# Kernel optimization log

Hardware: AMD Instinct MI355X
Metric: run time of the kernel (lower is better)

Reference implementation:

```python
import jax, jax.numpy as jnp
import numpy as np

B, S, D, H = 2, 2048, 1024, 16
HD = D // H
BAND_LOWER, BAND_UPPER = -1, 0  # tf.linalg.band_part args -> causal


def _causal_add_mask(seq_len):
    # 1 - band_part(ones, lower, upper); 1 where attention is DISALLOWED
    i = jnp.arange(seq_len)[:, None]
    j = jnp.arange(seq_len)[None, :]
    keep = jnp.ones((seq_len, seq_len), bool)
    if BAND_LOWER >= 0:
        keep = keep & ((i - j) <= BAND_LOWER)
    if BAND_UPPER >= 0:
        keep = keep & ((j - i) <= BAND_UPPER)
    return 1.0 - keep.astype(jnp.float32)


def setup_inputs() -> dict:
    key = jax.random.key(0)
    ks = jax.random.split(key, 5)
    scale = 1.0 / np.sqrt(D)
    return {
        "x": jax.random.normal(ks[0], (B, S, D), jnp.float32),
        "wq": jax.random.normal(ks[1], (D, D), jnp.float32) * scale,
        "bq": jnp.zeros((D,), jnp.float32),
        "wk": jax.random.normal(ks[2], (D, D), jnp.float32) * scale,
        "bk": jnp.zeros((D,), jnp.float32),
        "wv": jax.random.normal(ks[3], (D, D), jnp.float32) * scale,
        "bv": jnp.zeros((D,), jnp.float32),
        "wo": jax.random.normal(ks[4], (D, D), jnp.float32) * scale,
        "bo": jnp.zeros((D,), jnp.float32),
    }


def _split_heads(t):
    # [B, S, D] -> [B, H, S, HD]
    return t.reshape(B, S, H, HD).transpose(0, 2, 1, 3)


def reference(x, wq, bq, wk, bk, wv, bv, wo, bo):
    q = _split_heads(x @ wq + bq)
    k = _split_heads(x @ wk + bk)
    v = _split_heads(x @ wv + bv)
    mask = _causal_add_mask(S)  # [S, S], 1 where masked
    logits = jnp.einsum("bhqd,bhkd->bhqk", q, k) / jnp.sqrt(
        jnp.asarray(HD, jnp.float32)
    )
    logits = logits + mask * -1e9
    attn = jax.nn.softmax(logits, axis=-1)
    out = jnp.einsum("bhqk,bhkd->bhqd", attn, v)  # [B, H, S, HD]
    out = out.transpose(0, 2, 1, 3).reshape(B, S, D)
    return out @ wo + bo
```

## Files before the change

kernel.cpp:

```cpp
#include <hip/hip_runtime.h>

#define S_  2048
#define D_  1024
#define H_  16
#define HD_ 64
#define M_  4096
#define K_  1024
#define NEL 4194304

typedef short  bf16x8 __attribute__((ext_vector_type(8)));
typedef float  f32x4  __attribute__((ext_vector_type(4)));
typedef float  f32x16 __attribute__((ext_vector_type(16)));
typedef unsigned int   u32;
typedef unsigned int   u32x4v __attribute__((ext_vector_type(4)));
typedef unsigned short u16;
typedef unsigned short u16x4 __attribute__((ext_vector_type(4)));

#define MFMA16(c,a,b) (c) = __builtin_amdgcn_mfma_f32_16x16x32_bf16((a),(b),(c),0,0,0)
#define MFMA32(c,a,b) (c) = __builtin_amdgcn_mfma_f32_32x32x16_bf16((a),(b),(c),0,0,0)

#define QSCALE 0.18033688011112042f

__device__ __forceinline__ u16 f2bf(float f) {
    union { float f; unsigned u; } v; v.f = f;
    unsigned u = v.u;
    u += 0x7FFFu + ((u >> 16) & 1u);
    return (u16)(u >> 16);
}

__device__ __forceinline__ u32 cvtpk(float lo, float hi) {
    u32 r;
    asm("v_cvt_pk_bf16_f32 %0, %1, %2" : "=v"(r) : "v"(lo), "v"(hi));
    return r;
}

__device__ __forceinline__ void gload16(const void* g, void* l) {
    __builtin_amdgcn_global_load_lds(
        (const __attribute__((address_space(1))) unsigned*)g,
        (__attribute__((address_space(3))) unsigned*)l, 16, 0, 0);
}

__global__ __launch_bounds__(256) void cvt_x(const float* __restrict__ x,
                                             u16* __restrict__ xb) {
    const int i = (blockIdx.x * 256 + threadIdx.x) * 8;
    f32x4 a = *(const f32x4*)&x[i];
    f32x4 b = *(const f32x4*)&x[i + 4];
    u16 t[8];
#pragma unroll
    for (int j = 0; j < 4; ++j) { t[j] = f2bf(a[j]); t[4 + j] = f2bf(b[j]); }
    *(bf16x8*)&xb[i] = *(const bf16x8*)t;
}

__global__ __launch_bounds__(256) void cvt_w(const float* __restrict__ w0,
                                             const float* __restrict__ w1,
                                             const float* __restrict__ w2,
                                             const float* __restrict__ w3,
                                             u16* __restrict__ Wt) {
    __shared__ float T[64][65];
    const float* W = blockIdx.z == 0 ? w0 : blockIdx.z == 1 ? w1
                   : blockIdx.z == 2 ? w2 : w3;
    const int k0 = blockIdx.x * 64, n0 = blockIdx.y * 64;
    const int r  = threadIdx.x >> 2, c0 = (threadIdx.x & 3) * 16;
#pragma unroll
    for (int j = 0; j < 4; ++j)
        *(f32x4*)&T[r][c0 + j * 4] = *(const f32x4*)&W[(size_t)(k0 + r) * D_ + n0 + c0 + j * 4];
    __syncthreads();
    u16 tmp[16];
#pragma unroll
    for (int j = 0; j < 16; ++j) tmp[j] = f2bf(T[c0 + j][r]);
    u16* dst = Wt + ((size_t)blockIdx.z * 1024 + n0 + r) * K_ + k0 + c0;
    *(bf16x8*)dst       = *(const bf16x8*)tmp;
    *(bf16x8*)(dst + 8) = *(const bf16x8*)(tmp + 8);
}

template <int BM, int MODE>
__global__ __launch_bounds__(256) void gemm2(
    const u16* __restrict__ A, const u16* __restrict__ Bt,
    const float* __restrict__ bias, void* __restrict__ Out)
{
    __shared__ u16 As[BM * 32];
    __shared__ u16 Bs[128 * 32];
    const int tid = threadIdx.x, lane = tid & 63, wid = tid >> 6;
    const int lr = lane & 15, lg = lane >> 4;
    const int n0 = blockIdx.x * 128, m0 = blockIdx.y * BM;
    const int wm = (wid >> 1) * (BM / 2), wn = (wid & 1) * 64;
    const int lrow = lane >> 2, lch = lane & 3;

    f32x4 acc[BM / 32][4] = {};

    for (int k0 = 0; k0 < K_; k0 += 32) {
        __syncthreads();
#pragma unroll
        for (int t = 0; t < BM / 64; ++t) {
            const int row = wid * (BM / 4) + t * 16 + lrow;
            gload16(A + (size_t)(m0 + row) * K_ + k0 + lch * 8,
                    (u16*)As + row * 32 + lch * 8);
        }
#pragma unroll
        for (int t = 0; t < 2; ++t) {
            const int row = wid * 32 + t * 16 + lrow;
            gload16(Bt + (size_t)(n0 + row) * K_ + k0 + lch * 8,
                    (u16*)Bs + row * 32 + lch * 8);
        }
        __syncthreads();

        bf16x8 af[BM / 32], bf[4];
#pragma unroll
        for (int i = 0; i < BM / 32; ++i)
            af[i] = *(const bf16x8*)&As[(wm + i * 16 + lr) * 32 + lg * 8];
#pragma unroll
        for (int j = 0; j < 4; ++j)
            bf[j] = *(const bf16x8*)&Bs[(wn + j * 16 + lr) * 32 + lg * 8];
#pragma unroll
        for (int i = 0; i < BM / 32; ++i)
#pragma unroll
            for (int j = 0; j < 4; ++j) MFMA16(acc[i][j], af[i], bf[j]);
    }

#pragma unroll
    for (int i = 0; i < BM / 32; ++i) {
#pragma unroll
        for (int j = 0; j < 4; ++j) {
            const int n = n0 + wn + j * 16 + lr;
            const float bv = bias[n];
            const int m = m0 + wm + i * 16 + lg * 4;
            if constexpr (MODE == 0) {
                u16* qkv = (u16*)Out;
                const int which = n >> 10, nn = n & 1023;
                const int h = nn >> 6, hd = nn & 63;
                const int b = m >> 11, s = m & 2047;
                if (which == 2) {
                    u16x4 pk;
#pragma unroll
                    for (int r4 = 0; r4 < 4; ++r4) pk[r4] = f2bf(acc[i][j][r4] + bv);
                    *(u16x4*)&qkv[(size_t)2 * NEL +
                                  ((size_t)(b * H_ + h) * HD_ + hd) * S_ + s] = pk;
                } else {
                    const float sc = (which == 0) ? QSCALE : 1.0f;
                    const size_t bas = (size_t)which * NEL + (size_t)(b * H_ + h) * S_ * HD_;
#pragma unroll
                    for (int r4 = 0; r4 < 4; ++r4)
                        qkv[bas + (size_t)(s + r4) * HD_ + hd] =
                            f2bf((acc[i][j][r4] + bv) * sc);
                }
            } else {
                float* o = (float*)Out;
#pragma unroll
                for (int r4 = 0; r4 < 4; ++r4)
                    o[(size_t)(m + r4) * D_ + n] = acc[i][j][r4] + bv;
            }
        }
    }
}

__global__ __launch_bounds__(128) void attn5(
    const u16* __restrict__ Q, const u16* __restrict__ K,
    const u16* __restrict__ Vt, u16* __restrict__ CTX)
{
    __shared__ float OB[64][33];
    __shared__ float MB[64], LB[64];

    const int tid  = threadIdx.x;
    const int lane = tid & 63, wv = tid >> 6;
    const int lo = lane & 31, hi = lane >> 5;
    const int idx = blockIdx.x;
    const int bh  = idx & 31;
    const int qb  = 63 - (idx >> 5);
    const int wq0 = qb * 32;
    const size_t base  = (size_t)bh * S_ * HD_;
    const size_t vbase = (size_t)bh * HD_ * S_;

    bf16x8 qf[4];
#pragma unroll
    for (int ks = 0; ks < 4; ++ks)
        qf[ks] = *(const bf16x8*)&Q[base + (size_t)(wq0 + lo) * HD_ + ks * 16 + hi * 8];

    f32x16 acc[2] = {};
    float m_ = -1e30f, l_ = 0.f;
    const int nt = (wq0 >> 6) + 1;

    for (int t = wv; t < nt; t += 2) {
        const int kv0 = t * 64;
        const bool sub1 = (kv0 + 32 <= wq0 + 31);

        f32x16 cT[2];
#pragma unroll
        for (int i = 0; i < 16; ++i) { cT[0][i] = 0.f; cT[1][i] = 0.f; }
        __builtin_amdgcn_s_setprio(1);
#pragma unroll
        for (int ks = 0; ks < 4; ++ks) {
            bf16x8 kf = *(const bf16x8*)&K[base + (size_t)(kv0 + lo) * HD_ + ks * 16 + hi * 8];
            MFMA32(cT[0], kf, qf[ks]);
        }
        if (sub1) {
#pragma unroll
            for (int ks = 0; ks < 4; ++ks) {
                bf16x8 kf = *(const bf16x8*)&K[base + (size_t)(kv0 + 32 + lo) * HD_ + ks * 16 + hi * 8];
                MFMA32(cT[1], kf, qf[ks]);
            }
        }
        __builtin_amdgcn_s_setprio(0);

        bf16x8 vf[2][4];
#pragma unroll
        for (int dt = 0; dt < 2; ++dt)
#pragma unroll
            for (int ks = 0; ks < 4; ++ks)
                if (ks < 2 || sub1)
                    vf[dt][ks] = *(const bf16x8*)&Vt[vbase + (size_t)(dt * 32 + lo) * S_ +
                                                     kv0 + ks * 16 + hi * 8];

        if (kv0 + 63 > wq0) {
            const int qg = wq0 + lo;
#pragma unroll
            for (int tt = 0; tt < 2; ++tt)
#pragma unroll
                for (int r = 0; r < 16; ++r) {
                    const int kvg = kv0 + tt * 32 + (r & 3) + 8 * (r >> 2) + 4 * hi;
                    if (kvg > qg) cT[tt][r] = -1e9f;
                }
        }

        float m8[8];
#pragma unroll
        for (int i = 0; i < 8; ++i)
            m8[i] = fmaxf(fmaxf(cT[0][i], cT[0][i + 8]), fmaxf(cT[1][i], cT[1][i + 8]));
        float mx = fmaxf(fmaxf(fmaxf(m8[0], m8[1]), fmaxf(m8[2], m8[3])),
                         fmaxf(fmaxf(m8[4], m8[5]), fmaxf(m8[6], m8[7])));
        mx = fmaxf(mx, __shfl_xor(mx, 32));

        if (!__all(mx <= m_ + 11.5f)) {
            const float mn = fmaxf(m_, mx);
            const float al = exp2f(m_ - mn);
            m_ = mn; l_ *= al;
            float alr[16];
#pragma unroll
            for (int r = 0; r < 16; ++r)
                alr[r] = __shfl(al, (r & 3) + 8 * (r >> 2) + 4 * hi);
#pragma unroll
            for (int r = 0; r < 16; ++r) { acc[0][r] *= alr[r]; acc[1][r] *= alr[r]; }
        }

#pragma unroll
        for (int i = 0; i < 16; ++i) {
            cT[0][i] = exp2f(cT[0][i] - m_);
            cT[1][i] = exp2f(cT[1][i] - m_);
        }
        float s8[8];
#pragma unroll
        for (int i = 0; i < 8; ++i)
            s8[i] = (cT[0][i] + cT[0][i + 8]) + (cT[1][i] + cT[1][i + 8]);
        float ssum = ((s8[0] + s8[1]) + (s8[2] + s8[3])) +
                     ((s8[4] + s8[5]) + (s8[6] + s8[7]));
        ssum += __shfl_xor(ssum, 32);
        l_ += ssum;

        u32 pk[2][8];
#pragma unroll
        for (int tt = 0; tt < 2; ++tt)
#pragma unroll
            for (int w = 0; w < 8; ++w)
                pk[tt][w] = cvtpk(cT[tt][2 * w], cT[tt][2 * w + 1]);

#pragma unroll
        for (int ks = 0; ks < 4; ++ks) {
            if (ks < 2 || sub1) {
                const int tt = ks >> 1;
                const int ma = (2 * ks) & 3;
                const int mb = (2 * ks + 1) & 3;
                const u32 own0 = hi ? pk[tt][2 * mb]     : pk[tt][2 * ma];
                const u32 own1 = hi ? pk[tt][2 * mb + 1] : pk[tt][2 * ma + 1];
                const u32 snd0 = hi ? pk[tt][2 * ma]     : pk[tt][2 * mb];
                const u32 snd1 = hi ? pk[tt][2 * ma + 1] : pk[tt][2 * mb + 1];
                const u32 rcv0 = (u32)__shfl_xor((int)snd0, 32);
                const u32 rcv1 = (u32)__shfl_xor((int)snd1, 32);
                u32x4v afv;
                afv.x = hi ? rcv0 : own0;
                afv.y = hi ? rcv1 : own1;
                afv.z = hi ? own0 : rcv0;
                afv.w = hi ? own1 : rcv1;
                const bf16x8 af = __builtin_bit_cast(bf16x8, afv);
                __builtin_amdgcn_s_setprio(1);
                MFMA32(acc[0], af, vf[0][ks]);
                MFMA32(acc[1], af, vf[1][ks]);
                __builtin_amdgcn_s_setprio(0);
            }
        }
    }

    if (wv == 1) {
#pragma unroll
        for (int r = 0; r < 16; ++r) {
            OB[lane][r]      = acc[0][r];
            OB[lane][16 + r] = acc[1][r];
        }
        MB[lane] = m_;
        LB[lane] = l_;
    }
    __syncthreads();
    if (wv != 0) return;

    const float m1 = MB[lane], l1 = LB[lane];
    const float mM = fmaxf(m_, m1);
    const float a0 = exp2f(m_ - mM), a1 = exp2f(m1 - mM);
    l_ = l_ * a0 + l1 * a1;
    float a0r[16], a1r[16];
#pragma unroll
    for (int r = 0; r < 16; ++r) {
        const int rq = (r & 3) + 8 * (r >> 2) + 4 * hi;
        a0r[r] = __shfl(a0, rq);
        a1r[r] = __shfl(a1, rq);
    }
#pragma unroll
    for (int r = 0; r < 16; ++r) {
        acc[0][r] = acc[0][r] * a0r[r] + OB[lane][r]      * a1r[r];
        acc[1][r] = acc[1][r] * a0r[r] + OB[lane][16 + r] * a1r[r];
    }

    const float linv = 1.0f / l_;
    float lrr[16];
#pragma unroll
    for (int r = 0; r < 16; ++r)
        lrr[r] = __shfl(linv, (r & 3) + 8 * (r >> 2) + 4 * hi);
    const int b = bh >> 4, h = bh & 15;
#pragma unroll
    for (int r = 0; r < 16; ++r) {
        const int q = wq0 + (r & 3) + 8 * (r >> 2) + 4 * hi;
        u16* o = &CTX[(size_t)(b * S_ + q) * D_ + h * HD_ + lo];
        o[0]  = f2bf(acc[0][r] * lrr[r]);
        o[32] = f2bf(acc[1][r] * lrr[r]);
    }
}

extern "C" void kernel_launch(void* const* d_in, const int* in_sizes, int n_in,
                              void* d_out, int out_size, void* d_ws, size_t ws_size,
                              hipStream_t stream)
{
    const float* x  = (const float*)d_in[0];
    const float* wq = (const float*)d_in[1];
    const float* bq = (const float*)d_in[2];
    const float* wk = (const float*)d_in[3];
    const float* bk = (const float*)d_in[4];
    const float* wv = (const float*)d_in[5];
    const float* bv = (const float*)d_in[6];
    const float* wo = (const float*)d_in[7];
    const float* bo = (const float*)d_in[8];

    char* ws = (char*)d_ws;
    u16*   xb    = (u16*)ws;
    u16*   WtAll = (u16*)(ws + (size_t)8  * 1024 * 1024);
    u16*   qkv   = (u16*)(ws + (size_t)16 * 1024 * 1024);
    float* bias3 = (float*)(ws + (size_t)40 * 1024 * 1024);
    u16*   ctx   = xb;

    hipMemcpyAsync(bias3,          bq, D_ * 4, hipMemcpyDeviceToDevice, stream);
    hipMemcpyAsync(bias3 + D_,     bk, D_ * 4, hipMemcpyDeviceToDevice, stream);
    hipMemcpyAsync(bias3 + 2 * D_, bv, D_ * 4, hipMemcpyDeviceToDevice, stream);

    cvt_x<<<2048, 256, 0, stream>>>(x, xb);
    cvt_w<<<dim3(16, 16, 4), 256, 0, stream>>>(wq, wk, wv, wo, WtAll);

    gemm2<128, 0><<<dim3(24, 32), 256, 0, stream>>>(xb, WtAll, bias3, qkv);

    attn5<<<dim3(2048), 128, 0, stream>>>(qkv, qkv + NEL, qkv + 2 * (size_t)NEL, ctx);

    gemm2<64, 1><<<dim3(8, 64), 256, 0, stream>>>(ctx, WtAll + (size_t)3072 * K_, bo,
                                                  d_out);
}
```

Before: 158.1 us.

## Split attention KV loop across four waves and pass biases directly to GEMM

The attention kernel now runs four waves per block instead of two. The KV tiles are strided across the four waves, and the partial softmax/accumulator states are merged in two stages through shared memory. This gives each query block more parallelism and should shorten the long causal rows. The QKV GEMM also picks bq/bk/bv by column range, which removes the three device-to-device bias copies at launch. The cost is extra shared memory, extra syncs and merge work, and higher register pressure at 256 threads.

```diff
diff --git a/kernel.cpp b/kernel.cpp
--- a/kernel.cpp
+++ b/kernel.cpp
@@ -76,7 +76,8 @@
 template <int BM, int MODE>
 __global__ __launch_bounds__(256) void gemm2(
     const u16* __restrict__ A, const u16* __restrict__ Bt,
-    const float* __restrict__ bias, void* __restrict__ Out)
+    const float* __restrict__ b0, const float* __restrict__ b1,
+    const float* __restrict__ b2, void* __restrict__ Out)
 {
     __shared__ u16 As[BM * 32];
     __shared__ u16 Bs[128 * 32];
@@ -122,11 +123,12 @@
 #pragma unroll
         for (int j = 0; j < 4; ++j) {
             const int n = n0 + wn + j * 16 + lr;
-            const float bv = bias[n];
             const int m = m0 + wm + i * 16 + lg * 4;
             if constexpr (MODE == 0) {
+                const int which = n >> 10, nn = n & 1023;
+                const float* bp = which == 0 ? b0 : which == 1 ? b1 : b2;
+                const float bv = bp[nn];
                 u16* qkv = (u16*)Out;
-                const int which = n >> 10, nn = n & 1023;
                 const int h = nn >> 6, hd = nn & 63;
                 const int b = m >> 11, s = m & 2047;
                 if (which == 2) {
@@ -144,6 +146,7 @@
                             f2bf((acc[i][j][r4] + bv) * sc);
                 }
             } else {
+                const float bv = b0[n];
                 float* o = (float*)Out;
 #pragma unroll
                 for (int r4 = 0; r4 < 4; ++r4)
@@ -153,12 +156,12 @@
     }
 }
 
-__global__ __launch_bounds__(128) void attn5(
+__global__ __launch_bounds__(256, 4) void attn6(
     const u16* __restrict__ Q, const u16* __restrict__ K,
     const u16* __restrict__ Vt, u16* __restrict__ CTX)
 {
-    __shared__ float OB[64][33];
-    __shared__ float MB[64], LB[64];
+    __shared__ float OB[2][64][33];
+    __shared__ float MB[2][64], LB[2][64];
 
     const int tid  = threadIdx.x;
     const int lane = tid & 63, wv = tid >> 6;
@@ -179,7 +182,7 @@
     float m_ = -1e30f, l_ = 0.f;
     const int nt = (wq0 >> 6) + 1;
 
-    for (int t = wv; t < nt; t += 2) {
+    for (int t = wv; t < nt; t += 4) {
         const int kv0 = t * 64;
         const bool sub1 = (kv0 + 32 <= wq0 + 31);
 
@@ -288,33 +291,67 @@
         }
     }
 
+    if (wv >= 2) {
+        const int bb = wv - 2;
+#pragma unroll
+        for (int r = 0; r < 16; ++r) {
+            OB[bb][lane][r]      = acc[0][r];
+            OB[bb][lane][16 + r] = acc[1][r];
+        }
+        MB[bb][lane] = m_;
+        LB[bb][lane] = l_;
+    }
+    __syncthreads();
+    if (wv < 2) {
+        const int bb = wv;
+        const float m1 = MB[bb][lane], l1 = LB[bb][lane];
+        const float mM = fmaxf(m_, m1);
+        const float a0 = exp2f(m_ - mM), a1 = exp2f(m1 - mM);
+        m_ = mM;
+        l_ = l_ * a0 + l1 * a1;
+        float a0r[16], a1r[16];
+#pragma unroll
+        for (int r = 0; r < 16; ++r) {
+            const int rq = (r & 3) + 8 * (r >> 2) + 4 * hi;
+            a0r[r] = __shfl(a0, rq);
+            a1r[r] = __shfl(a1, rq);
+        }
+#pragma unroll
+        for (int r = 0; r < 16; ++r) {
+            acc[0][r] = acc[0][r] * a0r[r] + OB[bb][lane][r]      * a1r[r];
+            acc[1][r] = acc[1][r] * a0r[r] + OB[bb][lane][16 + r] * a1r[r];
+        }
+    }
+    __syncthreads();
     if (wv == 1) {
 #pragma unroll
         for (int r = 0; r < 16; ++r) {
-            OB[lane][r]      = acc[0][r];
-            OB[lane][16 + r] = acc[1][r];
-        }
-        MB[lane] = m_;
-        LB[lane] = l_;
+            OB[0][lane][r]      = acc[0][r];
+            OB[0][lane][16 + r] = acc[1][r];
+        }
+        MB[0][lane] = m_;
+        LB[0][lane] = l_;
     }
     __syncthreads();
     if (wv != 0) return;
 
-    const float m1 = MB[lane], l1 = LB[lane];
-    const float mM = fmaxf(m_, m1);
-    const float a0 = exp2f(m_ - mM), a1 = exp2f(m1 - mM);
-    l_ = l_ * a0 + l1 * a1;
-    float a0r[16], a1r[16];
-#pragma unroll
-    for (int r = 0; r < 16; ++r) {
-        const int rq = (r & 3) + 8 * (r >> 2) + 4 * hi;
-        a0r[r] = __shfl(a0, rq);
-        a1r[r] = __shfl(a1, rq);
-    }
-#pragma unroll
-    for (int r = 0; r < 16; ++r) {
-        acc[0][r] = acc[0][r] * a0r[r] + OB[lane][r]      * a1r[r];
-        acc[1][r] = acc[1][r] * a0r[r] + OB[lane][16 + r] * a1r[r];
+    {
+        const float m1 = MB[0][lane], l1 = LB[0][lane];
+        const float mM = fmaxf(m_, m1);
+        const float a0 = exp2f(m_ - mM), a1 = exp2f(m1 - mM);
+        l_ = l_ * a0 + l1 * a1;
+        float a0r[16], a1r[16];
+#pragma unroll
+        for (int r = 0; r < 16; ++r) {
+            const int rq = (r & 3) + 8 * (r >> 2) + 4 * hi;
+            a0r[r] = __shfl(a0, rq);
+            a1r[r] = __shfl(a1, rq);
+        }
+#pragma unroll
+        for (int r = 0; r < 16; ++r) {
+            acc[0][r] = acc[0][r] * a0r[r] + OB[0][lane][r]      * a1r[r];
+            acc[1][r] = acc[1][r] * a0r[r] + OB[0][lane][16 + r] * a1r[r];
+        }
     }
 
     const float linv = 1.0f / l_;
@@ -350,20 +387,15 @@
     u16*   xb    = (u16*)ws;
     u16*   WtAll = (u16*)(ws + (size_t)8  * 1024 * 1024);
     u16*   qkv   = (u16*)(ws + (size_t)16 * 1024 * 1024);
-    float* bias3 = (float*)(ws + (size_t)40 * 1024 * 1024);
     u16*   ctx   = xb;
-
-    hipMemcpyAsync(bias3,          bq, D_ * 4, hipMemcpyDeviceToDevice, stream);
-    hipMemcpyAsync(bias3 + D_,     bk, D_ * 4, hipMemcpyDeviceToDevice, stream);
-    hipMemcpyAsync(bias3 + 2 * D_, bv, D_ * 4, hipMemcpyDeviceToDevice, stream);
 
     cvt_x<<<2048, 256, 0, stream>>>(x, xb);
     cvt_w<<<dim3(16, 16, 4), 256, 0, stream>>>(wq, wk, wv, wo, WtAll);
 
-    gemm2<128, 0><<<dim3(24, 32), 256, 0, stream>>>(xb, WtAll, bias3, qkv);
-
-    attn5<<<dim3(2048), 128, 0, stream>>>(qkv, qkv + NEL, qkv + 2 * (size_t)NEL, ctx);
-
-    gemm2<64, 1><<<dim3(8, 64), 256, 0, stream>>>(ctx, WtAll + (size_t)3072 * K_, bo,
-                                                  d_out);
-}
+    gemm2<128, 0><<<dim3(24, 32), 256, 0, stream>>>(xb, WtAll, bq, bk, bv, qkv);
+
+    attn6<<<dim3(2048), 256, 0, stream>>>(qkv, qkv + NEL, qkv + 2 * (size_t)NEL, ctx);
+
+    gemm2<64, 1><<<dim3(8, 64), 256, 0, stream>>>(ctx, WtAll + (size_t)3072 * K_,
+                                                  bo, bo, bo, d_out);
+}
```

Result: slower. 335.0 us (+111.9%).
